# Optimization experiments

Measured on AMD Instinct MI355X. Metric: run time of the kernel, lower is better.

The kernel has to match this reference:

```python
import jax, jax.numpy as jnp
import numpy as np

N_NODES = 100000
N_EDGES = 1600000
IN_DIM = 48
HID = 128
BN_EPS = 1e-5


def _batchnorm(h, gamma, beta):
    # BatchNorm1d in training mode: batch mean, biased variance
    mu = jnp.mean(h, axis=0)
    var = jnp.mean(jnp.square(h - mu), axis=0)
    return (h - mu) * jax.lax.rsqrt(var + BN_EPS) * gamma + beta


def setup_inputs() -> dict:
    key = jax.random.key(0)
    ks = jax.random.split(key, 8)
    x = jax.random.normal(ks[0], (N_NODES, IN_DIM), dtype=jnp.float32)
    edge_index = jax.random.randint(ks[1], (2, N_EDGES), 0, N_NODES, dtype=jnp.int64)
    s1 = 1.0 / np.sqrt(IN_DIM)
    s2 = 1.0 / np.sqrt(HID)
    return {
        "x": x,
        "edge_index": edge_index,
        "W1": jax.random.uniform(ks[2], (HID, IN_DIM), jnp.float32, -s1, s1),
        "b1": jnp.zeros((HID,), jnp.float32),
        "g1": jnp.ones((HID,), jnp.float32),
        "be1": jnp.zeros((HID,), jnp.float32),
        "Wl": jax.random.uniform(ks[3], (HID, HID), jnp.float32, -s2, s2),
        "bl": jnp.zeros((HID,), jnp.float32),
        "Wr": jax.random.uniform(ks[4], (HID, HID), jnp.float32, -s2, s2),
        "g2": jnp.ones((HID,), jnp.float32),
        "be2": jnp.zeros((HID,), jnp.float32),
    }


def reference(x, edge_index, W1, b1, g1, be1, Wl, bl, Wr, g2, be2):
    # input projection: Linear -> BatchNorm -> ReLU
    h = x @ W1.T + b1                               # [N, HID]
    feat = jax.nn.relu(_batchnorm(h, g1, be1))      # [N, HID]

    # SAGEConv (mean aggregation): messages flow src -> dst
    src, dst = edge_index[0], edge_index[1]
    summed = jax.ops.segment_sum(feat[src], dst, num_segments=N_NODES)  # [N, HID]
    cnt = jax.ops.segment_sum(jnp.ones((N_EDGES,), jnp.float32), dst, num_segments=N_NODES)
    agg = summed / jnp.maximum(cnt, 1.0)[:, None]
    sage = agg @ Wl.T + bl + feat @ Wr.T            # lin_l(mean) + lin_r(self)

    out_feat = _batchnorm(sage, g2, be2)
    return (feat, out_feat)
```

## Files before the change

### kernel.cpp

```cpp
#include <hip/hip_runtime.h>
#include <hip/hip_bf16.h>

#define NN 100000
#define NE 1600000
#define INDIM 48
#define HID 128
#define K2 256
#define KP 64
#define BN_EPS 1e-5f

#define NBUK 782
#define BCAP 2816
#define CHUNK 8192

#define MT ((NN + 63) / 64)

typedef short s8v __attribute__((ext_vector_type(8)));
typedef float f4v __attribute__((ext_vector_type(4)));
typedef float f2v __attribute__((ext_vector_type(2)));

__device__ __forceinline__ unsigned short f2bf(float f) {
    __hip_bfloat16 b = __float2bfloat16(f);
    unsigned short u;
    __builtin_memcpy(&u, &b, 2);
    return u;
}
__device__ __forceinline__ float bflo(unsigned u) { return __uint_as_float(u << 16); }
__device__ __forceinline__ float bfhi(unsigned u) { return __uint_as_float(u & 0xffff0000u); }
__device__ __forceinline__ unsigned packbf(float lo, float hi) {
    return (unsigned)f2bf(lo) | ((unsigned)f2bf(hi) << 16);
}

__global__ __launch_bounds__(256) void k_prep(const float* __restrict__ Wl, const float* __restrict__ Wr,
                                              const float* __restrict__ W1,
                                              unsigned short* __restrict__ Wcat,
                                              unsigned short* __restrict__ W1b,
                                              int* __restrict__ bcur, float* __restrict__ stats) {
  int i = blockIdx.x * 256 + threadIdx.x;
  if (i < HID * K2) {
    int j = i >> 8, k = i & (K2 - 1);
    float v = (k < HID) ? Wl[j * HID + k] : Wr[j * HID + (k - HID)];
    Wcat[i] = f2bf(v);
  }
  int i2 = i - HID * K2;
  if (i2 >= 0 && i2 < HID * KP) {
    int j = i2 >> 6, k = i2 & (KP - 1);
    W1b[i2] = (k < INDIM) ? f2bf(W1[j * INDIM + k]) : (unsigned short)0;
  }
  int i3 = i2 - HID * KP;
  if (i3 >= 0 && i3 < NBUK) bcur[i3] = 0;
  int i4 = i3 - NBUK;
  if (i4 >= 0 && i4 < 4 * HID) stats[i4] = 0.f;
}

__global__ __launch_bounds__(256) void k_xcast(const float* __restrict__ x,
                                               unsigned short* __restrict__ xbf) {
  int i = blockIdx.x * 256 + threadIdx.x;
  if (i >= NN * 16) return;
  int r = i >> 4, c4 = (i & 15) << 2;
  ushort4 o = {0, 0, 0, 0};
  if (c4 < INDIM) {
    float4 v = *(const float4*)(x + (size_t)r * INDIM + c4);
    o.x = f2bf(v.x);
    o.y = f2bf(v.y);
    o.z = f2bf(v.z);
    o.w = f2bf(v.w);
  }
  *(ushort4*)(xbf + (size_t)r * KP + c4) = o;
}

__global__ __launch_bounds__(256) void k_proj_gemm(
    const unsigned short* __restrict__ xbf, const unsigned short* __restrict__ W1b,
    const float* __restrict__ b1, unsigned short* __restrict__ Abuf,
    float* __restrict__ colSum, float* __restrict__ colSq) {
  __shared__ __align__(16) unsigned short Bsh[HID][KP + 8];
  __shared__ float redS[4][HID], redQ[4][HID];
  int tid = threadIdx.x;
  for (int i = tid; i < HID * (KP / 8); i += 256) {
    int j = i >> 3, kg = (i & 7) << 3;
    *(s8v*)&Bsh[j][kg] = *(const s8v*)(W1b + (size_t)j * KP + kg);
  }
  __syncthreads();
  int w = tid >> 6, l = tid & 63;
  int m16 = l & 15, q = l >> 4;
  float bcol[8];
#pragma unroll
  for (int nt = 0; nt < 8; ++nt) bcol[nt] = b1[nt * 16 + m16];
  float ssum[8], ssq[8];
#pragma unroll
  for (int nt = 0; nt < 8; ++nt) { ssum[nt] = 0.f; ssq[nt] = 0.f; }
  f4v zero4 = {0.f, 0.f, 0.f, 0.f};
  s8v zero8 = {0, 0, 0, 0, 0, 0, 0, 0};
  for (int tile = blockIdx.x; tile < MT; tile += gridDim.x) {
    int row = tile * 64 + w * 16 + m16;
    bool rv = row < NN;
    f4v acc[8];
#pragma unroll
    for (int nt = 0; nt < 8; ++nt) acc[nt] = zero4;
#pragma unroll
    for (int kt = 0; kt < 2; ++kt) {
      s8v a = zero8;
      if (rv) a = *(const s8v*)(xbf + (size_t)row * KP + kt * 32 + q * 8);
#pragma unroll
      for (int nt = 0; nt < 8; ++nt) {
        s8v b = *(const s8v*)(&Bsh[nt * 16 + m16][kt * 32 + q * 8]);
        acc[nt] = __builtin_amdgcn_mfma_f32_16x16x32_bf16(a, b, acc[nt], 0, 0, 0);
      }
    }
    int rbase = tile * 64 + w * 16 + q * 4;
#pragma unroll
    for (int nt = 0; nt < 8; ++nt) {
      int col = nt * 16 + m16;
#pragma unroll
      for (int r4 = 0; r4 < 4; ++r4) {
        int rr = rbase + r4;
        if (rr < NN) {
          float v = acc[nt][r4] + bcol[nt];
          Abuf[(size_t)rr * K2 + HID + col] = f2bf(v);
          ssum[nt] += v;
          ssq[nt] = fmaf(v, v, ssq[nt]);
        }
      }
    }
  }
#pragma unroll
  for (int nt = 0; nt < 8; ++nt) {
    float s = ssum[nt], qq = ssq[nt];
    s += __shfl_xor(s, 16);
    s += __shfl_xor(s, 32);
    qq += __shfl_xor(qq, 16);
    qq += __shfl_xor(qq, 32);
    if (q == 0) {
      redS[w][nt * 16 + m16] = s;
      redQ[w][nt * 16 + m16] = qq;
    }
  }
  __syncthreads();
  if (tid < HID) {
    float s = redS[0][tid] + redS[1][tid] + redS[2][tid] + redS[3][tid];
    float qq = redQ[0][tid] + redQ[1][tid] + redQ[2][tid] + redQ[3][tid];
    atomicAdd(&colSum[tid], s);
    atomicAdd(&colSq[tid], qq);
  }
}

__global__ void k_bn_final(const float* __restrict__ sum, const float* __restrict__ sq,
                           const float* __restrict__ gamma, const float* __restrict__ beta,
                           float* __restrict__ av, float* __restrict__ bv) {
  int c = threadIdx.x;
  float mu = sum[c] * (1.0f / NN);
  float var = fmaxf(sq[c] * (1.0f / NN) - mu * mu, 0.f);
  float a = gamma[c] * rsqrtf(var + BN_EPS);
  av[c] = a;
  bv[c] = beta[c] - mu * a;
}

__global__ __launch_bounds__(256) void k_apply(float* __restrict__ feat,
                                               const float* __restrict__ av,
                                               const float* __restrict__ bv,
                                               unsigned short* __restrict__ A,
                                               unsigned char* __restrict__ feat8) {
  int i = blockIdx.x * 256 + threadIdx.x;
  if (i >= NN * 16) return;
  int r = i >> 4, c8 = (i & 15) << 3;
  unsigned short* ap = A + (size_t)r * K2 + HID + c8;
  uint4 hv = *(const uint4*)ap;
  float4 a0 = *(const float4*)(av + c8);
  float4 a1 = *(const float4*)(av + c8 + 4);
  float4 b0 = *(const float4*)(bv + c8);
  float4 b1 = *(const float4*)(bv + c8 + 4);
  float f0 = fmaxf(fmaf(bflo(hv.x), a0.x, b0.x), 0.f);
  float f1 = fmaxf(fmaf(bfhi(hv.x), a0.y, b0.y), 0.f);
  float f2 = fmaxf(fmaf(bflo(hv.y), a0.z, b0.z), 0.f);
  float f3 = fmaxf(fmaf(bfhi(hv.y), a0.w, b0.w), 0.f);
  float f4 = fmaxf(fmaf(bflo(hv.z), a1.x, b1.x), 0.f);
  float f5 = fmaxf(fmaf(bfhi(hv.z), a1.y, b1.y), 0.f);
  float f6 = fmaxf(fmaf(bflo(hv.w), a1.z, b1.z), 0.f);
  float f7 = fmaxf(fmaf(bfhi(hv.w), a1.w, b1.w), 0.f);
  float4 o0 = {f0, f1, f2, f3}, o1 = {f4, f5, f6, f7};
  *(float4*)(feat + (size_t)r * HID + c8) = o0;
  *(float4*)(feat + (size_t)r * HID + c8 + 4) = o1;
  uint4 ob;
  ob.x = packbf(f0, f1);
  ob.y = packbf(f2, f3);
  ob.z = packbf(f4, f5);
  ob.w = packbf(f6, f7);
  *(uint4*)ap = ob;
  unsigned p0 = __builtin_amdgcn_cvt_pk_fp8_f32(f0, f1, 0u, false);
  p0 = __builtin_amdgcn_cvt_pk_fp8_f32(f2, f3, p0, true);
  unsigned p1 = __builtin_amdgcn_cvt_pk_fp8_f32(f4, f5, 0u, false);
  p1 = __builtin_amdgcn_cvt_pk_fp8_f32(f6, f7, p1, true);
  uint2 o8 = {p0, p1};
  *(uint2*)(feat8 + (size_t)r * HID + c8) = o8;
}

__global__ __launch_bounds__(512) void k_bucket(const int* __restrict__ ei,
                                                int* __restrict__ bcur,
                                                unsigned int* __restrict__ bbuf) {
  __shared__ int cnt[1024];
  __shared__ int sc[2][1024];
  __shared__ int ofs[1024];
  __shared__ int lcur[1024];
  __shared__ int gbase[1024];
  __shared__ unsigned int stag[CHUNK];
  __shared__ unsigned short sbkt[CHUNK];
  int tid = threadIdx.x;
  int base = blockIdx.x * CHUNK;
  int lim = min(CHUNK, NE - base);
  cnt[tid] = 0;
  cnt[tid + 512] = 0;
  __syncthreads();
#pragma unroll
  for (int i = 0; i < CHUNK / 512; ++i) {
    int e = i * 512 + tid;
    if (e < lim) {
      int d = ei[NE + base + e];
      d = min(max(d, 0), NN - 1);
      atomicAdd(&cnt[d >> 7], 1);
    }
  }
  __syncthreads();
  sc[0][tid] = cnt[tid];
  sc[0][tid + 512] = cnt[tid + 512];
  __syncthreads();
  int pp = 0;
  for (int d = 1; d < 1024; d <<= 1) {
    int a0 = sc[pp][tid];
    int a1 = sc[pp][tid + 512];
    if (tid >= d) a0 += sc[pp][tid - d];
    a1 += sc[pp][tid + 512 - d];
    sc[pp ^ 1][tid] = a0;
    sc[pp ^ 1][tid + 512] = a1;
    __syncthreads();
    pp ^= 1;
  }
  ofs[tid] = sc[pp][tid] - cnt[tid];
  ofs[tid + 512] = sc[pp][tid + 512] - cnt[tid + 512];
  lcur[tid] = ofs[tid];
  lcur[tid + 512] = ofs[tid + 512];
  if (tid < NBUK) gbase[tid] = atomicAdd(&bcur[tid], cnt[tid]);
  if (tid + 512 < NBUK) gbase[tid + 512] = atomicAdd(&bcur[tid + 512], cnt[tid + 512]);
  __syncthreads();
#pragma unroll
  for (int i = 0; i < CHUNK / 512; ++i) {
    int e = i * 512 + tid;
    if (e < lim) {
      int s = ei[base + e];
      int d = ei[NE + base + e];
      s = min(max(s, 0), NN - 1);
      d = min(max(d, 0), NN - 1);
      int b = d >> 7;
      int pos = atomicAdd(&lcur[b], 1);
      stag[pos] = (unsigned)s | ((unsigned)(d & 127) << 17);
      sbkt[pos] = (unsigned short)b;
    }
  }
  __syncthreads();
  for (int s = tid; s < lim; s += 512) {
    int b = sbkt[s];
    int off = gbase[b] + (s - ofs[b]);
    if (off < BCAP) bbuf[(size_t)b * BCAP + off] = stag[s];
  }
}

__global__ __launch_bounds__(512) void k_bucket_agg(const unsigned int* __restrict__ bbuf,
                                                    const int* __restrict__ bcnt,
                                                    const unsigned char* __restrict__ feat8,
                                                    unsigned short* __restrict__ Abuf) {
  __shared__ unsigned int lcsr[BCAP];
  __shared__ int cnt[128], ofs[128], cur[128];
  __shared__ int sc[2][128];
  int tid = threadIdx.x;
  int b = blockIdx.x;
  int m = min(bcnt[b], BCAP);
  int n0 = b << 7;
  int nb = min(128, NN - n0);
  if (tid < 128) cnt[tid] = 0;
  __syncthreads();
  const unsigned int* bp = bbuf + (size_t)b * BCAP;
  for (int s = tid; s < m; s += 512) {
    unsigned p = bp[s];
    atomicAdd(&cnt[(p >> 17) & 127], 1);
  }
  __syncthreads();
  if (tid < 128) sc[0][tid] = cnt[tid];
  __syncthreads();
  int pp = 0;
  for (int d = 1; d < 128; d <<= 1) {
    if (tid < 128) {
      int v = sc[pp][tid];
      if (tid >= d) v += sc[pp][tid - d];
      sc[pp ^ 1][tid] = v;
    }
    __syncthreads();
    pp ^= 1;
  }
  if (tid < 128) {
    int o = sc[pp][tid] - cnt[tid];
    ofs[tid] = o;
    cur[tid] = o;
  }
  __syncthreads();
  for (int s = tid; s < m; s += 512) {
    unsigned p = bp[s];
    int ld = (p >> 17) & 127;
    int pos = atomicAdd(&cur[ld], 1);
    lcsr[pos] = p & 0x1FFFF;
  }
  __syncthreads();
  int lane = tid & 31;
  int g = tid >> 5;
  int half = (lane >> 3) & 3;
  int l8 = lane & 7;
  for (int ln = g; ln < nb; ln += 16) {
    int deg = cnt[ln], beg = ofs[ln];
    float ac[16];
#pragma unroll
    for (int i = 0; i < 16; ++i) ac[i] = 0.f;
#pragma unroll 2
    for (int j = 0; j < deg; j += 4) {
      int idx = j + half;
      uint4 v = {0u, 0u, 0u, 0u};
      if (idx < deg) {
        int s = lcsr[beg + idx];
        v = *(const uint4*)(feat8 + (size_t)s * HID + l8 * 16);
      }
      f2v d;
      d = __builtin_amdgcn_cvt_pk_f32_fp8(v.x, false); ac[0] += d.x;  ac[1] += d.y;
      d = __builtin_amdgcn_cvt_pk_f32_fp8(v.x, true);  ac[2] += d.x;  ac[3] += d.y;
      d = __builtin_amdgcn_cvt_pk_f32_fp8(v.y, false); ac[4] += d.x;  ac[5] += d.y;
      d = __builtin_amdgcn_cvt_pk_f32_fp8(v.y, true);  ac[6] += d.x;  ac[7] += d.y;
      d = __builtin_amdgcn_cvt_pk_f32_fp8(v.z, false); ac[8] += d.x;  ac[9] += d.y;
      d = __builtin_amdgcn_cvt_pk_f32_fp8(v.z, true);  ac[10] += d.x; ac[11] += d.y;
      d = __builtin_amdgcn_cvt_pk_f32_fp8(v.w, false); ac[12] += d.x; ac[13] += d.y;
      d = __builtin_amdgcn_cvt_pk_f32_fp8(v.w, true);  ac[14] += d.x; ac[15] += d.y;
    }
#pragma unroll
    for (int i = 0; i < 16; ++i) {
      ac[i] += __shfl_xor(ac[i], 8);
      ac[i] += __shfl_xor(ac[i], 16);
    }
    if (half == 0) {
      float inv = 1.f / fmaxf((float)deg, 1.f);
      uint4 o0, o1;
      o0.x = packbf(ac[0] * inv, ac[1] * inv);
      o0.y = packbf(ac[2] * inv, ac[3] * inv);
      o0.z = packbf(ac[4] * inv, ac[5] * inv);
      o0.w = packbf(ac[6] * inv, ac[7] * inv);
      o1.x = packbf(ac[8] * inv, ac[9] * inv);
      o1.y = packbf(ac[10] * inv, ac[11] * inv);
      o1.z = packbf(ac[12] * inv, ac[13] * inv);
      o1.w = packbf(ac[14] * inv, ac[15] * inv);
      unsigned short* op = Abuf + (size_t)(n0 + ln) * K2 + l8 * 16;
      *(uint4*)op = o0;
      *(uint4*)(op + 8) = o1;
    }
  }
}

__global__ __launch_bounds__(256) void k_gemm(
    const unsigned short* __restrict__ A, const unsigned short* __restrict__ Wcat,
    const float* __restrict__ bl, float* __restrict__ sage,
    float* __restrict__ colSum, float* __restrict__ colSq) {
  __shared__ __align__(16) unsigned short Bsh[64][264];
  __shared__ float redS[4][64], redQ[4][64];
  int tid = threadIdx.x;
  int ch = blockIdx.y;
  for (int i = tid; i < 64 * 32; i += 256) {
    int j = i >> 5;
    int kg = (i & 31) << 3;
    *(s8v*)&Bsh[j][kg] = *(const s8v*)(Wcat + ((size_t)(ch * 64 + j)) * K2 + kg);
  }
  __syncthreads();
  int w = tid >> 6, l = tid & 63;
  int m16 = l & 15, q = l >> 4;
  float ssum[4] = {0.f, 0.f, 0.f, 0.f}, ssq[4] = {0.f, 0.f, 0.f, 0.f};
  f4v zero4 = {0.f, 0.f, 0.f, 0.f};
  s8v zero8 = {0, 0, 0, 0, 0, 0, 0, 0};
  for (int tile = blockIdx.x; tile < MT; tile += gridDim.x) {
    int row = tile * 64 + w * 16 + m16;
    bool rv = row < NN;
    f4v acc[4];
#pragma unroll
    for (int nt = 0; nt < 4; ++nt) acc[nt] = zero4;
#pragma unroll
    for (int kt = 0; kt < 8; ++kt) {
      s8v a = zero8;
      if (rv) a = *(const s8v*)(A + (size_t)row * K2 + kt * 32 + q * 8);
#pragma unroll
      for (int nt = 0; nt < 4; ++nt) {
        s8v bfr = *(const s8v*)(&Bsh[nt * 16 + m16][kt * 32 + q * 8]);
        acc[nt] = __builtin_amdgcn_mfma_f32_16x16x32_bf16(a, bfr, acc[nt], 0, 0, 0);
      }
    }
    int rbase = tile * 64 + w * 16 + q * 4;
#pragma unroll
    for (int nt = 0; nt < 4; ++nt) {
      int col = ch * 64 + nt * 16 + m16;
      float bv = bl[col];
#pragma unroll
      for (int r4 = 0; r4 < 4; ++r4) {
        int rr = rbase + r4;
        if (rr < NN) {
          float v = acc[nt][r4] + bv;
          sage[(size_t)rr * HID + col] = v;
          ssum[nt] += v;
          ssq[nt] = fmaf(v, v, ssq[nt]);
        }
      }
    }
  }
#pragma unroll
  for (int nt = 0; nt < 4; ++nt) {
    float s = ssum[nt], qq = ssq[nt];
    s += __shfl_xor(s, 16);
    s += __shfl_xor(s, 32);
    qq += __shfl_xor(qq, 16);
    qq += __shfl_xor(qq, 32);
    if (q == 0) {
      redS[w][nt * 16 + m16] = s;
      redQ[w][nt * 16 + m16] = qq;
    }
  }
  __syncthreads();
  if (tid < 64) {
    float s = redS[0][tid] + redS[1][tid] + redS[2][tid] + redS[3][tid];
    float qq = redQ[0][tid] + redQ[1][tid] + redQ[2][tid] + redQ[3][tid];
    atomicAdd(&colSum[ch * 64 + tid], s);
    atomicAdd(&colSq[ch * 64 + tid], qq);
  }
}

__global__ __launch_bounds__(256) void k_bn_apply(float* __restrict__ sage,
                                                  const float* __restrict__ av,
                                                  const float* __restrict__ bv) {
  int i = blockIdx.x * 256 + threadIdx.x;
  if (i < NN * HID / 4) {
    float4 s = ((const float4*)sage)[i];
    int c = (i * 4) & (HID - 1);
    float4 a = *(const float4*)(av + c);
    float4 b = *(const float4*)(bv + c);
    float4 o;
    o.x = fmaf(s.x, a.x, b.x);
    o.y = fmaf(s.y, a.y, b.y);
    o.z = fmaf(s.z, a.z, b.z);
    o.w = fmaf(s.w, a.w, b.w);
    ((float4*)sage)[i] = o;
  }
}

extern "C" void kernel_launch(void* const* d_in, const int* in_sizes, int n_in,
                              void* d_out, int out_size, void* d_ws, size_t ws_size,
                              hipStream_t stream) {
  const float* x   = (const float*)d_in[0];
  const int*   ei  = (const int*)d_in[1];
  const float* W1  = (const float*)d_in[2];
  const float* b1  = (const float*)d_in[3];
  const float* g1  = (const float*)d_in[4];
  const float* be1 = (const float*)d_in[5];
  const float* Wl  = (const float*)d_in[6];
  const float* bl  = (const float*)d_in[7];
  const float* Wr  = (const float*)d_in[8];
  const float* g2  = (const float*)d_in[9];
  const float* be2 = (const float*)d_in[10];

  float* feat_out = (float*)d_out;
  float* sage     = (float*)d_out + (size_t)NN * HID;

  size_t off = 0;
  auto alloc = [&](size_t bytes) -> void* {
    void* p = (char*)d_ws + off;
    off += (bytes + 255) & ~(size_t)255;
    return p;
  };
  unsigned short* Abuf = (unsigned short*)alloc((size_t)NN * K2 * 2);
  unsigned char*  feat8 = (unsigned char*)alloc((size_t)NN * HID);
  unsigned int*   bbuf = (unsigned int*)alloc((size_t)NBUK * BCAP * 4);
  int*            bcur = (int*)alloc((size_t)NBUK * 4);
  float*          stats = (float*)alloc(8 * HID * 4);
  float* colSum1 = stats;
  float* colSq1  = stats + HID;
  float* colSum2 = stats + 2 * HID;
  float* colSq2  = stats + 3 * HID;
  float* a1v     = stats + 4 * HID;
  float* b1v     = stats + 5 * HID;
  float* a2v     = stats + 6 * HID;
  float* b2v     = stats + 7 * HID;
  unsigned short* Wcat = (unsigned short*)alloc((size_t)HID * K2 * 2);
  unsigned short* W1b  = (unsigned short*)alloc((size_t)HID * KP * 2);
  unsigned short* xbf  = (unsigned short*)alloc((size_t)NN * KP * 2);

  int prep_n = HID * K2 + HID * KP + NBUK + 4 * HID;
  k_prep<<<(prep_n + 255) / 256, 256, 0, stream>>>(Wl, Wr, W1, Wcat, W1b, bcur, stats);
  k_xcast<<<(NN * 16 + 255) / 256, 256, 0, stream>>>(x, xbf);
  k_bucket<<<(NE + CHUNK - 1) / CHUNK, 512, 0, stream>>>(ei, bcur, bbuf);
  k_proj_gemm<<<512, 256, 0, stream>>>(xbf, W1b, b1, Abuf, colSum1, colSq1);
  k_bn_final<<<1, HID, 0, stream>>>(colSum1, colSq1, g1, be1, a1v, b1v);
  k_apply<<<(NN * 16 + 255) / 256, 256, 0, stream>>>(feat_out, a1v, b1v, Abuf, feat8);
  k_bucket_agg<<<NBUK, 512, 0, stream>>>(bbuf, bcur, feat8, Abuf);
  k_gemm<<<dim3(512, 2), 256, 0, stream>>>(Abuf, Wcat, bl, sage, colSum2, colSq2);
  k_bn_final<<<1, HID, 0, stream>>>(colSum2, colSq2, g2, be2, a2v, b2v);
  k_bn_apply<<<(NN * HID / 4 + 255) / 256, 256, 0, stream>>>(sage, a2v, b2v);
}
```

Baseline: 307.3 us.

## Store pre-BN SAGE output as bf16, widen GEMM tile to full 128 columns, merge prep kernels

The final GEMM now writes its pre-normalization output as bf16 to a workspace buffer, and the BN apply pass reads that buffer and writes fp32 to the output. This replaces the fp32 read-modify-write of the output and cuts intermediate traffic. The GEMM uses 512-thread blocks that each cover 128 rows and all 128 columns, one tile per block, so the A matrix is read once instead of twice across two column halves. The weight prep and x-cast kernels are merged into one launch. The risk is extra rounding error from keeping the intermediate in bf16 before normalization.

```diff
diff --git a/kernel.cpp b/kernel.cpp
--- a/kernel.cpp
+++ b/kernel.cpp
@@ -14,6 +14,7 @@
 #define CHUNK 8192
 
 #define MT ((NN + 63) / 64)
+#define MT2 ((NN + 127) / 128)
 
 typedef short s8v __attribute__((ext_vector_type(8)));
 typedef float f4v __attribute__((ext_vector_type(4)));
@@ -31,12 +32,26 @@
     return (unsigned)f2bf(lo) | ((unsigned)f2bf(hi) << 16);
 }
 
-__global__ __launch_bounds__(256) void k_prep(const float* __restrict__ Wl, const float* __restrict__ Wr,
-                                              const float* __restrict__ W1,
-                                              unsigned short* __restrict__ Wcat,
-                                              unsigned short* __restrict__ W1b,
-                                              int* __restrict__ bcur, float* __restrict__ stats) {
+__global__ __launch_bounds__(256) void k_xcast(const float* __restrict__ x,
+                                               unsigned short* __restrict__ xbf,
+                                               const float* __restrict__ Wl, const float* __restrict__ Wr,
+                                               const float* __restrict__ W1,
+                                               unsigned short* __restrict__ Wcat,
+                                               unsigned short* __restrict__ W1b,
+                                               int* __restrict__ bcur, float* __restrict__ stats) {
   int i = blockIdx.x * 256 + threadIdx.x;
+  if (i < NN * 16) {
+    int r = i >> 4, c4 = (i & 15) << 2;
+    ushort4 o = {0, 0, 0, 0};
+    if (c4 < INDIM) {
+      float4 v = *(const float4*)(x + (size_t)r * INDIM + c4);
+      o.x = f2bf(v.x);
+      o.y = f2bf(v.y);
+      o.z = f2bf(v.z);
+      o.w = f2bf(v.w);
+    }
+    *(ushort4*)(xbf + (size_t)r * KP + c4) = o;
+  }
   if (i < HID * K2) {
     int j = i >> 8, k = i & (K2 - 1);
     float v = (k < HID) ? Wl[j * HID + k] : Wr[j * HID + (k - HID)];
@@ -51,22 +66,6 @@
   if (i3 >= 0 && i3 < NBUK) bcur[i3] = 0;
   int i4 = i3 - NBUK;
   if (i4 >= 0 && i4 < 4 * HID) stats[i4] = 0.f;
-}
-
-__global__ __launch_bounds__(256) void k_xcast(const float* __restrict__ x,
-                                               unsigned short* __restrict__ xbf) {
-  int i = blockIdx.x * 256 + threadIdx.x;
-  if (i >= NN * 16) return;
-  int r = i >> 4, c4 = (i & 15) << 2;
-  ushort4 o = {0, 0, 0, 0};
-  if (c4 < INDIM) {
-    float4 v = *(const float4*)(x + (size_t)r * INDIM + c4);
-    o.x = f2bf(v.x);
-    o.y = f2bf(v.y);
-    o.z = f2bf(v.z);
-    o.w = f2bf(v.w);
-  }
-  *(ushort4*)(xbf + (size_t)r * KP + c4) = o;
 }
 
 __global__ __launch_bounds__(256) void k_proj_gemm(
@@ -358,60 +357,60 @@
   }
 }
 
-__global__ __launch_bounds__(256) void k_gemm(
+__global__ __launch_bounds__(512) void k_gemm(
     const unsigned short* __restrict__ A, const unsigned short* __restrict__ Wcat,
-    const float* __restrict__ bl, float* __restrict__ sage,
+    const float* __restrict__ bl, unsigned short* __restrict__ sageb,
     float* __restrict__ colSum, float* __restrict__ colSq) {
-  __shared__ __align__(16) unsigned short Bsh[64][264];
-  __shared__ float redS[4][64], redQ[4][64];
+  __shared__ __align__(16) unsigned short Bsh[HID][264];
+  __shared__ float redS[8][HID], redQ[8][HID];
   int tid = threadIdx.x;
-  int ch = blockIdx.y;
-  for (int i = tid; i < 64 * 32; i += 256) {
+  for (int i = tid; i < HID * 32; i += 512) {
     int j = i >> 5;
     int kg = (i & 31) << 3;
-    *(s8v*)&Bsh[j][kg] = *(const s8v*)(Wcat + ((size_t)(ch * 64 + j)) * K2 + kg);
+    *(s8v*)&Bsh[j][kg] = *(const s8v*)(Wcat + (size_t)j * K2 + kg);
   }
   __syncthreads();
   int w = tid >> 6, l = tid & 63;
   int m16 = l & 15, q = l >> 4;
-  float ssum[4] = {0.f, 0.f, 0.f, 0.f}, ssq[4] = {0.f, 0.f, 0.f, 0.f};
+  int tile = blockIdx.x;
+  int row = tile * 128 + w * 16 + m16;
+  bool rv = row < NN;
   f4v zero4 = {0.f, 0.f, 0.f, 0.f};
   s8v zero8 = {0, 0, 0, 0, 0, 0, 0, 0};
-  for (int tile = blockIdx.x; tile < MT; tile += gridDim.x) {
-    int row = tile * 64 + w * 16 + m16;
-    bool rv = row < NN;
-    f4v acc[4];
-#pragma unroll
-    for (int nt = 0; nt < 4; ++nt) acc[nt] = zero4;
-#pragma unroll
-    for (int kt = 0; kt < 8; ++kt) {
-      s8v a = zero8;
-      if (rv) a = *(const s8v*)(A + (size_t)row * K2 + kt * 32 + q * 8);
-#pragma unroll
-      for (int nt = 0; nt < 4; ++nt) {
-        s8v bfr = *(const s8v*)(&Bsh[nt * 16 + m16][kt * 32 + q * 8]);
-        acc[nt] = __builtin_amdgcn_mfma_f32_16x16x32_bf16(a, bfr, acc[nt], 0, 0, 0);
+  f4v acc[8];
+#pragma unroll
+  for (int nt = 0; nt < 8; ++nt) acc[nt] = zero4;
+#pragma unroll
+  for (int kt = 0; kt < 8; ++kt) {
+    s8v a = zero8;
+    if (rv) a = *(const s8v*)(A + (size_t)row * K2 + kt * 32 + q * 8);
+#pragma unroll
+    for (int nt = 0; nt < 8; ++nt) {
+      s8v bfr = *(const s8v*)(&Bsh[nt * 16 + m16][kt * 32 + q * 8]);
+      acc[nt] = __builtin_amdgcn_mfma_f32_16x16x32_bf16(a, bfr, acc[nt], 0, 0, 0);
+    }
+  }
+  int rbase = tile * 128 + w * 16 + q * 4;
+  float ssum[8], ssq[8];
+#pragma unroll
+  for (int nt = 0; nt < 8; ++nt) { ssum[nt] = 0.f; ssq[nt] = 0.f; }
+#pragma unroll
+  for (int nt = 0; nt < 8; ++nt) {
+    int col = nt * 16 + m16;
+    float bv = bl[col];
+#pragma unroll
+    for (int r4 = 0; r4 < 4; ++r4) {
+      int rr = rbase + r4;
+      if (rr < NN) {
+        float v = acc[nt][r4] + bv;
+        sageb[(size_t)rr * HID + col] = f2bf(v);
+        ssum[nt] += v;
+        ssq[nt] = fmaf(v, v, ssq[nt]);
       }
     }
-    int rbase = tile * 64 + w * 16 + q * 4;
-#pragma unroll
-    for (int nt = 0; nt < 4; ++nt) {
-      int col = ch * 64 + nt * 16 + m16;
-      float bv = bl[col];
-#pragma unroll
-      for (int r4 = 0; r4 < 4; ++r4) {
-        int rr = rbase + r4;
-        if (rr < NN) {
-          float v = acc[nt][r4] + bv;
-          sage[(size_t)rr * HID + col] = v;
-          ssum[nt] += v;
-          ssq[nt] = fmaf(v, v, ssq[nt]);
-        }
-      }
-    }
-  }
-#pragma unroll
-  for (int nt = 0; nt < 4; ++nt) {
+  }
+#pragma unroll
+  for (int nt = 0; nt < 8; ++nt) {
     float s = ssum[nt], qq = ssq[nt];
     s += __shfl_xor(s, 16);
     s += __shfl_xor(s, 32);
@@ -423,30 +422,38 @@
     }
   }
   __syncthreads();
-  if (tid < 64) {
-    float s = redS[0][tid] + redS[1][tid] + redS[2][tid] + redS[3][tid];
-    float qq = redQ[0][tid] + redQ[1][tid] + redQ[2][tid] + redQ[3][tid];
-    atomicAdd(&colSum[ch * 64 + tid], s);
-    atomicAdd(&colSq[ch * 64 + tid], qq);
-  }
-}
-
-__global__ __launch_bounds__(256) void k_bn_apply(float* __restrict__ sage,
+  if (tid < HID) {
+    float s = 0.f, qq = 0.f;
+#pragma unroll
+    for (int ww = 0; ww < 8; ++ww) { s += redS[ww][tid]; qq += redQ[ww][tid]; }
+    atomicAdd(&colSum[tid], s);
+    atomicAdd(&colSq[tid], qq);
+  }
+}
+
+__global__ __launch_bounds__(256) void k_bn_apply(const unsigned short* __restrict__ sageb,
+                                                  float* __restrict__ out,
                                                   const float* __restrict__ av,
                                                   const float* __restrict__ bv) {
   int i = blockIdx.x * 256 + threadIdx.x;
-  if (i < NN * HID / 4) {
-    float4 s = ((const float4*)sage)[i];
-    int c = (i * 4) & (HID - 1);
-    float4 a = *(const float4*)(av + c);
-    float4 b = *(const float4*)(bv + c);
-    float4 o;
-    o.x = fmaf(s.x, a.x, b.x);
-    o.y = fmaf(s.y, a.y, b.y);
-    o.z = fmaf(s.z, a.z, b.z);
-    o.w = fmaf(s.w, a.w, b.w);
-    ((float4*)sage)[i] = o;
-  }
+  if (i >= NN * 16) return;
+  int r = i >> 4, c8 = (i & 15) << 3;
+  uint4 sv = *(const uint4*)(sageb + (size_t)r * HID + c8);
+  float4 a0 = *(const float4*)(av + c8);
+  float4 a1 = *(const float4*)(av + c8 + 4);
+  float4 b0 = *(const float4*)(bv + c8);
+  float4 b1 = *(const float4*)(bv + c8 + 4);
+  float4 o0, o1;
+  o0.x = fmaf(bflo(sv.x), a0.x, b0.x);
+  o0.y = fmaf(bfhi(sv.x), a0.y, b0.y);
+  o0.z = fmaf(bflo(sv.y), a0.z, b0.z);
+  o0.w = fmaf(bfhi(sv.y), a0.w, b0.w);
+  o1.x = fmaf(bflo(sv.z), a1.x, b1.x);
+  o1.y = fmaf(bfhi(sv.z), a1.y, b1.y);
+  o1.z = fmaf(bflo(sv.w), a1.z, b1.z);
+  o1.w = fmaf(bfhi(sv.w), a1.w, b1.w);
+  *(float4*)(out + (size_t)r * HID + c8) = o0;
+  *(float4*)(out + (size_t)r * HID + c8 + 4) = o1;
 }
 
 extern "C" void kernel_launch(void* const* d_in, const int* in_sizes, int n_in,
@@ -465,7 +472,7 @@
   const float* be2 = (const float*)d_in[10];
 
   float* feat_out = (float*)d_out;
-  float* sage     = (float*)d_out + (size_t)NN * HID;
+  float* out2     = (float*)d_out + (size_t)NN * HID;
 
   size_t off = 0;
   auto alloc = [&](size_t bytes) -> void* {
@@ -475,6 +482,7 @@
   };
   unsigned short* Abuf = (unsigned short*)alloc((size_t)NN * K2 * 2);
   unsigned char*  feat8 = (unsigned char*)alloc((size_t)NN * HID);
+  unsigned short* sageb = (unsigned short*)alloc((size_t)NN * HID * 2);
   unsigned int*   bbuf = (unsigned int*)alloc((size_t)NBUK * BCAP * 4);
   int*            bcur = (int*)alloc((size_t)NBUK * 4);
   float*          stats = (float*)alloc(8 * HID * 4);
@@ -490,15 +498,13 @@
   unsigned short* W1b  = (unsigned short*)alloc((size_t)HID * KP * 2);
   unsigned short* xbf  = (unsigned short*)alloc((size_t)NN * KP * 2);
 
-  int prep_n = HID * K2 + HID * KP + NBUK + 4 * HID;
-  k_prep<<<(prep_n + 255) / 256, 256, 0, stream>>>(Wl, Wr, W1, Wcat, W1b, bcur, stats);
-  k_xcast<<<(NN * 16 + 255) / 256, 256, 0, stream>>>(x, xbf);
+  k_xcast<<<(NN * 16 + 255) / 256, 256, 0, stream>>>(x, xbf, Wl, Wr, W1, Wcat, W1b, bcur, stats);
   k_bucket<<<(NE + CHUNK - 1) / CHUNK, 512, 0, stream>>>(ei, bcur, bbuf);
   k_proj_gemm<<<512, 256, 0, stream>>>(xbf, W1b, b1, Abuf, colSum1, colSq1);
   k_bn_final<<<1, HID, 0, stream>>>(colSum1, colSq1, g1, be1, a1v, b1v);
   k_apply<<<(NN * 16 + 255) / 256, 256, 0, stream>>>(feat_out, a1v, b1v, Abuf, feat8);
   k_bucket_agg<<<NBUK, 512, 0, stream>>>(bbuf, bcur, feat8, Abuf);
-  k_gemm<<<dim3(512, 2), 256, 0, stream>>>(Abuf, Wcat, bl, sage, colSum2, colSq2);
+  k_gemm<<<MT2, 512, 0, stream>>>(Abuf, Wcat, bl, sageb, colSum2, colSq2);
   k_bn_final<<<1, HID, 0, stream>>>(colSum2, colSq2, g2, be2, a2v, b2v);
-  k_bn_apply<<<(NN * HID / 4 + 255) / 256, 256, 0, stream>>>(sage, a2v, b2v);
-}
+  k_bn_apply<<<(NN * 16 + 255) / 256, 256, 0, stream>>>(sageb, out2, a2v, b2v);
+}
```

Measured after the change: 294.3 us. -4.2%, faster.
